# Kernel tuning notes

Measured on AMD Instinct MI355X. Metric: run time of the kernel, lower is better.

Reference implementation:

```python
import jax, jax.numpy as jnp
import numpy as np

ALPHA = 0.2  # leaky-relu negative slope


def setup_inputs() -> dict:
    key = jax.random.key(0)
    k1, k2, k3, k4 = jax.random.split(key, 4)
    bs, L, D, Fin, Fout = 4, 20000, 16, 128, 128
    x = jax.random.normal(k1, (bs, L, Fin), dtype=jnp.float32)
    adj = jax.random.randint(k2, (bs, L, D), 0, L, dtype=jnp.int64)
    # xavier_normal-ish init for W [Fin, Fout] and a [2*Fout, 1]
    W = jax.random.normal(k3, (Fin, Fout), dtype=jnp.float32) * (1.414 * np.sqrt(2.0 / (Fin + Fout))).astype(np.float32)
    a = jax.random.normal(k4, (2 * Fout, 1), dtype=jnp.float32) * (1.414 * np.sqrt(2.0 / (2 * Fout + 1))).astype(np.float32)
    return {"x": x, "adj": adj, "W": W, "a": a}


def reference(x, adj, W, a):
    Fout = W.shape[1]
    # gather fixed-degree neighbor features: [bs, L, D, Fin]
    nbr = jax.vmap(lambda xb, ab: xb[ab])(x, adj)
    h = jnp.matmul(nbr, W)  # [bs, L, D, Fout]
    # a is applied to cat([h_neighbor, h_center]); split it instead of concatenating
    a1 = a[:Fout, 0]
    a2 = a[Fout:, 0]
    # h[:, :, 0, :] is the center node (first neighbor slot, repeat_interleave in torch)
    e = jnp.einsum('bldf,f->bld', h, a1) + jnp.einsum('blf,f->bl', h[:, :, 0, :], a2)[..., None]
    attn = jax.nn.softmax(jax.nn.leaky_relu(e, ALPHA), axis=-1)  # softmax over D
    out = jnp.einsum('bld,bldf->blf', attn, h)  # weighted aggregate [bs, L, Fout]
    return jax.nn.elu(out)  # concat=True branch
```

## Files before the change

### kernel.cpp

```cpp
#include <hip/hip_runtime.h>
#include <hip/hip_bf16.h>

#define LSEQ 20000
#define DEG  16
#define F    128
#define ALPHA 0.2f

typedef __bf16 bf16x8 __attribute__((ext_vector_type(8)));
typedef float  f32x4  __attribute__((ext_vector_type(4)));

__global__ __launch_bounds__(256) void gat_wt(const float* __restrict__ W,
                                              const float* __restrict__ a,
                                              __hip_bfloat16* __restrict__ wt,
                                              float* __restrict__ wa)
{
    const int t = blockIdx.x * 256 + threadIdx.x;
    for (int i = t; i < F * F; i += 16 * 256) {
        const int k = i >> 7, n = i & (F - 1);
        wt[n * F + k] = __float2bfloat16(W[i]);
    }
    if (blockIdx.x == 0 && threadIdx.x < F) {
        const int k = threadIdx.x;
        float acc1 = 0.f, acc2 = 0.f;
        for (int n = 0; n < F; ++n) {
            const float w = W[k * F + n];
            acc1 = fmaf(w, a[n],     acc1);
            acc2 = fmaf(w, a[F + n], acc2);
        }
        wa[k]     = acc1;
        wa[F + k] = acc2;
    }
}

__global__ __launch_bounds__(256) void gat_gemm(const float* __restrict__ x,
                                                const __hip_bfloat16* __restrict__ wt,
                                                const float* __restrict__ wa,
                                                __hip_bfloat16* __restrict__ y16,
                                                float* __restrict__ s1,
                                                float* __restrict__ s2)
{
    const int lane = threadIdx.x & 63;
    const int wv   = (blockIdx.x * 256 + threadIdx.x) >> 6;
    const int i0   = wv * 16;
    const int m    = lane & 15;
    const int q    = lane >> 4;

    const float* xr = x + (size_t)(i0 + m) * F + q * 8;
    float4 xf[8];
    #pragma unroll
    for (int kt = 0; kt < 4; ++kt) {
        xf[2*kt]   = *reinterpret_cast<const float4*>(xr + kt * 32);
        xf[2*kt+1] = *reinterpret_cast<const float4*>(xr + kt * 32 + 4);
    }

    float p1 = 0.f, p2 = 0.f;
    {
        const float* w1p = wa + q * 8;
        const float* w2p = wa + F + q * 8;
        #pragma unroll
        for (int kt = 0; kt < 4; ++kt) {
            const float4 u0 = *reinterpret_cast<const float4*>(w1p + kt * 32);
            const float4 u1 = *reinterpret_cast<const float4*>(w1p + kt * 32 + 4);
            const float4 v0 = *reinterpret_cast<const float4*>(w2p + kt * 32);
            const float4 v1 = *reinterpret_cast<const float4*>(w2p + kt * 32 + 4);
            const float4 xa = xf[2*kt], xb = xf[2*kt+1];
            p1 = fmaf(xa.x,u0.x,p1); p1 = fmaf(xa.y,u0.y,p1);
            p1 = fmaf(xa.z,u0.z,p1); p1 = fmaf(xa.w,u0.w,p1);
            p1 = fmaf(xb.x,u1.x,p1); p1 = fmaf(xb.y,u1.y,p1);
            p1 = fmaf(xb.z,u1.z,p1); p1 = fmaf(xb.w,u1.w,p1);
            p2 = fmaf(xa.x,v0.x,p2); p2 = fmaf(xa.y,v0.y,p2);
            p2 = fmaf(xa.z,v0.z,p2); p2 = fmaf(xa.w,v0.w,p2);
            p2 = fmaf(xb.x,v1.x,p2); p2 = fmaf(xb.y,v1.y,p2);
            p2 = fmaf(xb.z,v1.z,p2); p2 = fmaf(xb.w,v1.w,p2);
        }
    }
    p1 += __shfl_xor(p1, 16); p1 += __shfl_xor(p1, 32);
    p2 += __shfl_xor(p2, 16); p2 += __shfl_xor(p2, 32);
    if (lane < 16) {
        s1[i0 + m] = p1;
        s2[i0 + m] = p2;
    }

    bf16x8 bfr[4];
    #pragma unroll
    for (int kt = 0; kt < 4; ++kt) {
        const float4 qa = xf[2*kt], qb = xf[2*kt+1];
        bf16x8 f;
        f[0] = (__bf16)qa.x; f[1] = (__bf16)qa.y; f[2] = (__bf16)qa.z; f[3] = (__bf16)qa.w;
        f[4] = (__bf16)qb.x; f[5] = (__bf16)qb.y; f[6] = (__bf16)qb.z; f[7] = (__bf16)qb.w;
        bfr[kt] = f;
    }

    #pragma unroll
    for (int ct = 0; ct < 8; ++ct) {
        union { uint4 u; bf16x8 v; } afr[4];
        const __hip_bfloat16* wrow = wt + (size_t)(ct * 16 + m) * F + q * 8;
        #pragma unroll
        for (int kt = 0; kt < 4; ++kt)
            afr[kt].u = *reinterpret_cast<const uint4*>(wrow + kt * 32);

        f32x4 acc = {0.f, 0.f, 0.f, 0.f};
        #pragma unroll
        for (int kt = 0; kt < 4; ++kt)
            acc = __builtin_amdgcn_mfma_f32_16x16x32_bf16(afr[kt].v, bfr[kt], acc, 0, 0, 0);

        union { uint2 u; __hip_bfloat162 h[2]; } pk;
        pk.h[0] = __float22bfloat162_rn(make_float2(acc[0], acc[1]));
        pk.h[1] = __float22bfloat162_rn(make_float2(acc[2], acc[3]));
        *reinterpret_cast<uint2*>(y16 + (size_t)(i0 + m) * F + ct * 16 + q * 4) = pk.u;
    }
}

__global__ __launch_bounds__(256) void gat_attn(const int* __restrict__ adj,
                                                const __hip_bfloat16* __restrict__ y16,
                                                const float* __restrict__ s1,
                                                const float* __restrict__ s2,
                                                float* __restrict__ out)
{
    const int lane  = threadIdx.x & 63;
    const int wid   = threadIdx.x >> 6;
    const int x8    = blockIdx.x & 7;
    const int j     = blockIdx.x >> 3;
    const int batch = x8 >> 1;
    const int nb    = j * 2 + (x8 & 1);
    const int gl    = batch * LSEQ + nb * 4 + wid;
    const int base  = batch * LSEQ;

    const int* adjp = adj + (size_t)gl * DEG;
    int av = (lane < DEG) ? adjp[lane] : 0;

    float sv = (lane < DEG) ? s1[base + av] : 0.f;
    const int a0 = __builtin_amdgcn_readlane(av, 0);
    const float e = sv + s2[base + a0];
    const float t = e > 0.f ? e : ALPHA * e;

    float m = t;
    #pragma unroll
    for (int off = 8; off; off >>= 1) m = fmaxf(m, __shfl_xor(m, off));
    float w = (lane < DEG) ? __expf(t - m) : 0.f;
    float p = w;
    #pragma unroll
    for (int off = 8; off; off >>= 1) p += __shfl_xor(p, off);
    const float attn = w / p;

    unsigned int v[DEG];
    #pragma unroll
    for (int d = 0; d < DEG; ++d) {
        const int nbr = __builtin_amdgcn_readlane(av, d);
        const unsigned int* row =
            reinterpret_cast<const unsigned int*>(y16 + ((size_t)(base + nbr) << 7));
        v[d] = row[lane];
    }

    float accx = 0.f, accy = 0.f;
    #pragma unroll
    for (int d = 0; d < DEG; ++d) {
        const float ad = __uint_as_float(
            __builtin_amdgcn_readlane(__float_as_uint(attn), d));
        accx = fmaf(ad, __uint_as_float(v[d] << 16),          accx);
        accy = fmaf(ad, __uint_as_float(v[d] & 0xffff0000u),  accy);
    }
    const float ox = accx > 0.f ? accx : __expf(accx) - 1.f;
    const float oy = accy > 0.f ? accy : __expf(accy) - 1.f;
    *reinterpret_cast<float2*>(out + (size_t)gl * F + lane * 2) = make_float2(ox, oy);
}

extern "C" void kernel_launch(void* const* d_in, const int* in_sizes, int n_in,
                              void* d_out, int out_size, void* d_ws, size_t ws_size,
                              hipStream_t stream) {
    const float* x   = (const float*)d_in[0];
    const int*   adj = (const int*)d_in[1];
    const float* W   = (const float*)d_in[2];
    const float* a   = (const float*)d_in[3];
    float* out = (float*)d_out;

    const int BL = in_sizes[0] / F;

    __hip_bfloat16* y16 = (__hip_bfloat16*)d_ws;
    float* s1 = (float*)((char*)d_ws + (size_t)BL * F * sizeof(__hip_bfloat16));
    float* s2 = s1 + BL;
    __hip_bfloat16* wt = (__hip_bfloat16*)(s2 + BL);
    float* wa = (float*)(wt + F * F);

    gat_wt  <<<16, 256, 0, stream>>>(W, a, wt, wa);
    gat_gemm<<<BL / 64, 256, 0, stream>>>(x, wt, wa, y16, s1, s2);
    gat_attn<<<BL / 4, 256, 0, stream>>>(adj, y16, s1, s2, out);
}
```

Baseline: 150.7 us.

## Process four nodes per wavefront in attention kernel using all 64 lanes

Each wavefront now handles four destination nodes instead of one, so all 64 lanes load adjacency and score values and run the softmax in 16-lane segments instead of leaving 48 lanes idle. The neighbor-row gathers for two nodes are issued together before the accumulation, raising memory-level parallelism, and the grid shrinks by a factor of four. The cost is higher register pressure from holding 32 gathered values at once. Block-to-batch mapping assumes LSEQ divides evenly by 64 nodes per block pair.

```diff
diff --git a/kernel.cpp b/kernel.cpp
--- a/kernel.cpp
+++ b/kernel.cpp
@@ -122,47 +122,68 @@
     const int x8    = blockIdx.x & 7;
     const int j     = blockIdx.x >> 3;
     const int batch = x8 >> 1;
-    const int nb    = j * 2 + (x8 & 1);
-    const int gl    = batch * LSEQ + nb * 4 + wid;
+    const int grp   = j * 2 + (x8 & 1);
     const int base  = batch * LSEQ;
-
-    const int* adjp = adj + (size_t)gl * DEG;
-    int av = (lane < DEG) ? adjp[lane] : 0;
-
-    float sv = (lane < DEG) ? s1[base + av] : 0.f;
-    const int a0 = __builtin_amdgcn_readlane(av, 0);
-    const float e = sv + s2[base + a0];
+    const int g0    = base + grp * 16 + wid * 4;
+
+    const int av = adj[(size_t)g0 * DEG + lane];
+
+    const float sv = s1[base + av];
+    const int d = lane & 15;
+    float s2l = (d == 0) ? s2[base + av] : 0.f;
+    const float s2v = __shfl(s2l, lane & 48);
+    const float e = sv + s2v;
     const float t = e > 0.f ? e : ALPHA * e;
 
     float m = t;
     #pragma unroll
-    for (int off = 8; off; off >>= 1) m = fmaxf(m, __shfl_xor(m, off));
-    float w = (lane < DEG) ? __expf(t - m) : 0.f;
+    for (int off = 1; off < 16; off <<= 1) m = fmaxf(m, __shfl_xor(m, off));
+    const float w = __expf(t - m);
     float p = w;
     #pragma unroll
-    for (int off = 8; off; off >>= 1) p += __shfl_xor(p, off);
+    for (int off = 1; off < 16; off <<= 1) p += __shfl_xor(p, off);
     const float attn = w / p;
 
-    unsigned int v[DEG];
-    #pragma unroll
-    for (int d = 0; d < DEG; ++d) {
-        const int nbr = __builtin_amdgcn_readlane(av, d);
-        const unsigned int* row =
-            reinterpret_cast<const unsigned int*>(y16 + ((size_t)(base + nbr) << 7));
-        v[d] = row[lane];
-    }
-
-    float accx = 0.f, accy = 0.f;
-    #pragma unroll
-    for (int d = 0; d < DEG; ++d) {
-        const float ad = __uint_as_float(
-            __builtin_amdgcn_readlane(__float_as_uint(attn), d));
-        accx = fmaf(ad, __uint_as_float(v[d] << 16),          accx);
-        accy = fmaf(ad, __uint_as_float(v[d] & 0xffff0000u),  accy);
-    }
-    const float ox = accx > 0.f ? accx : __expf(accx) - 1.f;
-    const float oy = accy > 0.f ? accy : __expf(accy) - 1.f;
-    *reinterpret_cast<float2*>(out + (size_t)gl * F + lane * 2) = make_float2(ox, oy);
+    #pragma unroll
+    for (int n = 0; n < 4; n += 2) {
+        unsigned int v0[DEG], v1[DEG];
+        #pragma unroll
+        for (int dd = 0; dd < DEG; ++dd) {
+            const int i0 = __builtin_amdgcn_readlane(av, n * 16 + dd);
+            v0[dd] = reinterpret_cast<const unsigned int*>(
+                         y16 + ((size_t)(base + i0) << 7))[lane];
+        }
+        #pragma unroll
+        for (int dd = 0; dd < DEG; ++dd) {
+            const int i1 = __builtin_amdgcn_readlane(av, (n + 1) * 16 + dd);
+            v1[dd] = reinterpret_cast<const unsigned int*>(
+                         y16 + ((size_t)(base + i1) << 7))[lane];
+        }
+
+        float ax0 = 0.f, ay0 = 0.f, ax1 = 0.f, ay1 = 0.f;
+        #pragma unroll
+        for (int dd = 0; dd < DEG; ++dd) {
+            const float ad0 = __uint_as_float(__builtin_amdgcn_readlane(
+                                  __float_as_uint(attn), n * 16 + dd));
+            union { unsigned int u; __hip_bfloat162 h; } c0; c0.u = v0[dd];
+            const float2 f0 = __bfloat1622float2(c0.h);
+            ax0 = fmaf(ad0, f0.x, ax0); ay0 = fmaf(ad0, f0.y, ay0);
+
+            const float ad1 = __uint_as_float(__builtin_amdgcn_readlane(
+                                  __float_as_uint(attn), (n + 1) * 16 + dd));
+            union { unsigned int u; __hip_bfloat162 h; } c1; c1.u = v1[dd];
+            const float2 f1 = __bfloat1622float2(c1.h);
+            ax1 = fmaf(ad1, f1.x, ax1); ay1 = fmaf(ad1, f1.y, ay1);
+        }
+        const float ox0 = ax0 > 0.f ? ax0 : __expf(ax0) - 1.f;
+        const float oy0 = ay0 > 0.f ? ay0 : __expf(ay0) - 1.f;
+        *reinterpret_cast<float2*>(out + (size_t)(g0 + n) * F + lane * 2)
+            = make_float2(ox0, oy0);
+        const float ox1 = ax1 > 0.f ? ax1 : __expf(ax1) - 1.f;
+        const float oy1 = ay1 > 0.f ? ay1 : __expf(ay1) - 1.f;
+        *reinterpret_cast<float2*>(out + (size_t)(g0 + n + 1) * F + lane * 2)
+            = make_float2(ox1, oy1);
+    }
 }
 
 extern "C" void kernel_launch(void* const* d_in, const int* in_sizes, int n_in,
@@ -184,5 +205,5 @@
 
     gat_wt  <<<16, 256, 0, stream>>>(W, a, wt, wa);
     gat_gemm<<<BL / 64, 256, 0, stream>>>(x, wt, wa, y16, s1, s2);
-    gat_attn<<<BL / 4, 256, 0, stream>>>(adj, y16, s1, s2, out);
-}
+    gat_attn<<<BL / 16, 256, 0, stream>>>(adj, y16, s1, s2, out);
+}
```

After: 148.6 us. About the same (-1.4%).
